# Performance work log

Measured on AMD Instinct MI355X. Metric: run time of the kernel, lower is better.

The kernel has to match this reference:

```python
import jax, jax.numpy as jnp
import numpy as np

B, T, O, D, H = 8, 256, 16, 512, 8
HD = D // H
EPS = 1e-5


def setup_inputs() -> dict:
    key = jax.random.key(0)
    ks = jax.random.split(key, 12)
    s = 1.0 / np.sqrt(D)
    inp = {
        "organ_states": jax.random.normal(ks[0], (B, T, O, D), dtype=jnp.float32),
        "organ_mask": jax.random.randint(ks[1], (B, T, O), 0, 2) > 0,
        "Wq": jax.random.uniform(ks[2], (D, D), jnp.float32, -s, s),
        "bq": jnp.zeros((D,), jnp.float32),
        "Wk": jax.random.uniform(ks[3], (D, D), jnp.float32, -s, s),
        "bk": jnp.zeros((D,), jnp.float32),
        "Wv": jax.random.uniform(ks[4], (D, D), jnp.float32, -s, s),
        "bv": jnp.zeros((D,), jnp.float32),
        "Wo": jax.random.uniform(ks[5], (D, D), jnp.float32, -s, s),
        "bo": jnp.zeros((D,), jnp.float32),
        "gamma": jnp.ones((D,), jnp.float32),
        "beta": jnp.zeros((D,), jnp.float32),
    }
    return inp


def reference(organ_states, organ_mask, Wq, bq, Wk, bk, Wv, bv, Wo, bo, gamma, beta):
    x = organ_states  # (B, T, O, D)
    b, t, o, d = x.shape

    def heads(y):  # (B,T,O,D) -> (B,O,H,T,HD)
        return y.reshape(b, t, o, H, HD).transpose(0, 2, 3, 1, 4)

    q = heads(jnp.einsum('btod,de->btoe', x, Wq) + bq)
    k = heads(jnp.einsum('btod,de->btoe', x, Wk) + bk)
    v = heads(jnp.einsum('btod,de->btoe', x, Wv) + bv)

    scores = jnp.einsum('bohqd,bohkd->bohqk', q, k) / np.sqrt(HD).astype(np.float32)
    # key mask: (B,T,O) -> (B,O,1,1,T)
    mk = organ_mask.transpose(0, 2, 1)[:, :, None, None, :]
    scores = jnp.where(mk, scores, -jnp.inf)
    attn = jax.nn.softmax(scores, axis=-1)
    attn = jnp.where(mk, attn, 0.0)

    att = jnp.einsum('bohqk,bohkd->bohqd', attn, v)  # (B,O,H,T,HD)
    att = att.transpose(0, 3, 1, 2, 4).reshape(b, t, o, d)  # (B,T,O,D)

    out = jnp.einsum('btod,de->btoe', att, Wo) + bo
    res = out + x
    mu = jnp.mean(res, axis=-1, keepdims=True)
    var = jnp.mean(jnp.square(res - mu), axis=-1, keepdims=True)
    y = (res - mu) / jnp.sqrt(var + EPS) * gamma + beta
    y = y * organ_mask[..., None].astype(y.dtype)
    return y
```

## Files before the change

kernel.cpp:

```cpp
#include <hip/hip_runtime.h>


typedef __attribute__((ext_vector_type(8))) short bf16x8;
typedef __attribute__((ext_vector_type(4))) float f32x4;

#define MFMA16(a, b, c) __builtin_amdgcn_mfma_f32_16x16x32_bf16((a), (b), (c), 0, 0, 0)

__device__ __forceinline__ unsigned short f2bf(float f) {
  unsigned int u = __builtin_bit_cast(unsigned int, f);
  u += 0x7fffu + ((u >> 16) & 1u);
  return (unsigned short)(u >> 16);
}

__device__ __forceinline__ void gload_lds16(const void* g, void* lds) {
  __builtin_amdgcn_global_load_lds((__attribute__((address_space(1))) void*)g,
                                   (__attribute__((address_space(3))) void*)lds,
                                   16, 0, 0);
}

#define WS_XB   0ull
#define WS_WT   33554432ull
#define WS_Q    35651584ull
#define WS_K    69206016ull
#define WS_V    102760448ull
#define WS_MASK 136314880ull

__global__ void k_cvt_x(const float* __restrict__ x, unsigned short* __restrict__ xb) {
  int i = blockIdx.x * 256 + threadIdx.x;
  float4 v = ((const float4*)x)[i];
  ushort4 o;
  o.x = f2bf(v.x); o.y = f2bf(v.y); o.z = f2bf(v.z); o.w = f2bf(v.w);
  ((ushort4*)xb)[i] = o;
}

__global__ void k_prep_w(const float* __restrict__ Wq, const float* __restrict__ Wk,
                         const float* __restrict__ Wv, const float* __restrict__ Wo,
                         unsigned short* __restrict__ Wt) {
  __shared__ float tl[64][65];
  const float* src = blockIdx.z == 0 ? Wq : blockIdx.z == 1 ? Wk : blockIdx.z == 2 ? Wv : Wo;
  const int d0 = blockIdx.x * 64, e0 = blockIdx.y * 64;
  const int tid = threadIdx.x;
  {
    const int dr = tid >> 2, ec = (tid & 3) * 16;
    const float4* srow = (const float4*)(src + (size_t)(d0 + dr) * 512 + e0 + ec);
#pragma unroll
    for (int j = 0; j < 4; ++j) {
      float4 v = srow[j];
      tl[dr][ec + j * 4 + 0] = v.x;
      tl[dr][ec + j * 4 + 1] = v.y;
      tl[dr][ec + j * 4 + 2] = v.z;
      tl[dr][ec + j * 4 + 3] = v.w;
    }
  }
  __syncthreads();
  const int dd0 = (tid & 7) * 8;
#pragma unroll
  for (int i = 0; i < 2; ++i) {
    int e = i * 32 + (tid >> 3);
    bf16x8 ob;
#pragma unroll
    for (int j = 0; j < 8; ++j) ob[j] = (short)f2bf(tl[dd0 + j][e]);
    *(bf16x8*)(Wt + ((size_t)blockIdx.z * 512 + e0 + e) * 512 + d0 + dd0) = ob;
  }
}

__global__ void k_prep_mask(const void* __restrict__ mraw, unsigned char* __restrict__ mout) {
  const unsigned int* u = (const unsigned int*)mraw;
  int lane = threadIdx.x & 63;
  int packed = __any(u[lane] > 1u);
  int idx = blockIdx.x * 256 + threadIdx.x;
  unsigned char m;
  if (packed) m = ((const unsigned char*)mraw)[idx] ? 1 : 0;
  else        m = u[idx] ? 1 : 0;
  mout[idx] = m;
}

__global__ __launch_bounds__(256) void k_qkv(
    const unsigned short* __restrict__ Xb, const unsigned short* __restrict__ Wt,
    const float* __restrict__ bq, const float* __restrict__ bk, const float* __restrict__ bv,
    unsigned short* __restrict__ Qb, unsigned short* __restrict__ Kb, unsigned short* __restrict__ Vb) {
  __shared__ char sm[32768];
  const int tid = threadIdx.x, l = tid & 63, w = tid >> 6;
  const int lane15 = l & 15, quad = l >> 4;
  const int flat = blockIdx.x;
  const int mtile = flat / 12, yb = flat % 12;
  const int which = yb >> 2, ntile = yb & 3;
  const int rbase = mtile * 128;
  const char* xg = (const char*)Xb + (size_t)rbase * 1024;
  const char* wgp = (const char*)(Wt + ((size_t)which * 512 + ntile * 128) * 512);
  const int wr = w >> 1, wc = w & 1;
  const int srow = tid >> 3;
  const int c16 = (tid & 7) * 16;
  char* const abase = sm;
  char* const bbase = sm + 16384;
  f32x4 acc[4][4] = {};
  for (int ks = 0; ks < 8; ++ks) {
    __syncthreads();
#pragma unroll
    for (int i = 0; i < 4; ++i) {
      int row = i * 32 + srow;
      int swz = c16 ^ ((row & 7) << 4);
      gload_lds16(xg + (size_t)row * 1024 + ks * 128 + swz, abase + i * 4096 + w * 1024);
      gload_lds16(wgp + (size_t)row * 1024 + ks * 128 + swz, bbase + i * 4096 + w * 1024);
    }
    __syncthreads();
#pragma unroll
    for (int kc = 0; kc < 2; ++kc) {
      bf16x8 af[4], bfr[4];
#pragma unroll
      for (int mt = 0; mt < 4; ++mt) {
        int row = wr * 64 + mt * 16 + lane15;
        af[mt] = *(const bf16x8*)(abase + row * 128 + ((kc * 64 + quad * 16) ^ ((row & 7) << 4)));
      }
#pragma unroll
      for (int nt = 0; nt < 4; ++nt) {
        int col = wc * 64 + nt * 16 + lane15;
        bfr[nt] = *(const bf16x8*)(bbase + col * 128 + ((kc * 64 + quad * 16) ^ ((col & 7) << 4)));
      }
#pragma unroll
      for (int mt = 0; mt < 4; ++mt)
#pragma unroll
        for (int nt = 0; nt < 4; ++nt)
          acc[mt][nt] = MFMA16(af[mt], bfr[nt], acc[mt][nt]);
    }
  }
  const float* bias = (which == 0) ? bq : (which == 1) ? bk : bv;
  unsigned short* dst = (which == 0) ? Qb : (which == 1) ? Kb : Vb;
  const int h = ntile * 2 + wc;
#pragma unroll
  for (int mt = 0; mt < 4; ++mt) {
#pragma unroll
    for (int reg = 0; reg < 4; ++reg) {
      int r = rbase + wr * 64 + mt * 16 + quad * 4 + reg;
      int b = r >> 12, t = (r >> 4) & 255, o = r & 15;
      size_t base_bt = (size_t)((b * 16 + o) * 8 + h) * 16384 + (size_t)t * 64;
#pragma unroll
      for (int nt = 0; nt < 4; ++nt) {
        int hd = nt * 16 + lane15;
        dst[base_bt + hd] = f2bf(acc[mt][nt][reg] + bias[h * 64 + hd]);
      }
    }
  }
}

__global__ __launch_bounds__(512, 2) void k_attn(
    const unsigned short* __restrict__ Qb, const unsigned short* __restrict__ Kb,
    const unsigned short* __restrict__ Vb, const unsigned char* __restrict__ Mc,
    unsigned short* __restrict__ att) {
  __shared__ char sm[99328];
  const int tid = threadIdx.x, l = tid & 63, w = tid >> 6;
  const int lane15 = l & 15, quad = l >> 4;
  const int bid = blockIdx.x;
  const int h = bid & 7, o = (bid >> 3) & 15, b = bid >> 7;
  const size_t head = (size_t)((b * 16 + o) * 8 + h) * 16384;
  const unsigned short* qh = Qb + head;
  const char* kg = (const char*)(Kb + head);
  const unsigned short* vh = Vb + head;

  {
    const int srow = tid >> 3;
    const int c16 = (tid & 7) * 16;
    char* kdst = sm + w * 1024;
#pragma unroll
    for (int i = 0; i < 4; ++i) {
      int t = i * 64 + srow;
      gload_lds16(kg + (size_t)t * 128 + (c16 ^ ((t & 7) << 4)), kdst + i * 8192);
    }
  }
  const int q0 = w * 32;
  bf16x8 qf[2][2];
#pragma unroll
  for (int mt = 0; mt < 2; ++mt)
#pragma unroll
    for (int kc = 0; kc < 2; ++kc)
      qf[mt][kc] = *(const bf16x8*)(qh + (size_t)(q0 + mt * 16 + lane15) * 64 + kc * 32 + quad * 8);
  unsigned short vreg[32];
  {
    const int hd = tid & 63, tq = tid >> 6;
#pragma unroll
    for (int i = 0; i < 4; ++i)
#pragma unroll
      for (int j = 0; j < 8; ++j)
        vreg[i * 8 + j] = vh[(size_t)(tq * 32 + i * 8 + j) * 64 + hd];
  }
  float* maskb = (float*)(sm + 98304);
  if (tid < 256)
    maskb[tid] = Mc[(size_t)(b * 256 + tid) * 16 + o] ? 0.0f : -43280.0f;
  {
    const int hd = tid & 63, tq = tid >> 6;
    const int rowb = 32768 + hd * 512;
    const int swz = (hd & 7) << 4;
#pragma unroll
    for (int i = 0; i < 4; ++i) {
      bf16x8 pk;
#pragma unroll
      for (int j = 0; j < 8; ++j) pk[j] = (short)vreg[i * 8 + j];
      int t0 = tq * 32 + i * 8;
      *(bf16x8*)(sm + rowb + ((t0 * 2) ^ swz)) = pk;
    }
  }
  __syncthreads();

  f32x4 sacc[2][16] = {};
#pragma unroll
  for (int c = 0; c < 4; ++c) {
#pragma unroll
    for (int kc = 0; kc < 2; ++kc) {
      bf16x8 kf[4];
#pragma unroll
      for (int nt = 0; nt < 4; ++nt) {
        int t = c * 64 + nt * 16 + lane15;
        int byt = t * 128 + ((kc * 64 + quad * 16) ^ ((t & 7) << 4));
        kf[nt] = *(const bf16x8*)(sm + byt);
      }
#pragma unroll
      for (int mt = 0; mt < 2; ++mt)
#pragma unroll
        for (int nt = 0; nt < 4; ++nt)
          sacc[mt][c * 4 + nt] = MFMA16(qf[mt][kc], kf[nt], sacc[mt][c * 4 + nt]);
    }
  }

  float biasv[16];
#pragma unroll
  for (int g = 0; g < 16; ++g) biasv[g] = maskb[g * 16 + lane15];
  float inv[2][4];
#pragma unroll
  for (int mt = 0; mt < 2; ++mt) {
#pragma unroll
    for (int reg = 0; reg < 4; ++reg) {
      float v[16];
#pragma unroll
      for (int g = 0; g < 16; ++g)
        v[g] = sacc[mt][g][reg] * 0.18033688f + biasv[g];
      float m = v[0];
#pragma unroll
      for (int g = 1; g < 16; ++g) m = fmaxf(m, v[g]);
#pragma unroll
      for (int d = 1; d < 16; d <<= 1) m = fmaxf(m, __shfl_xor(m, d));
      float rs = 0.f;
#pragma unroll
      for (int g = 0; g < 16; ++g) {
        float p = __builtin_amdgcn_exp2f(v[g] - m);
        sacc[mt][g][reg] = p;
        rs += p;
      }
#pragma unroll
      for (int d = 1; d < 16; d <<= 1) rs += __shfl_xor(rs, d);
      inv[mt][reg] = 1.0f / rs;
    }
  }

  char* pb = sm + 65536 + w * 4096;
  f32x4 pv[2][4] = {};
#pragma unroll
  for (int c = 0; c < 4; ++c) {
#pragma unroll
    for (int mt = 0; mt < 2; ++mt)
#pragma unroll
      for (int nt = 0; nt < 4; ++nt)
#pragma unroll
        for (int reg = 0; reg < 4; ++reg) {
          int qrow = mt * 16 + quad * 4 + reg;
          int byt = (qrow * 128 + (nt * 16 + lane15) * 2) ^ ((qrow & 7) << 4);
          *(unsigned short*)(pb + byt) = f2bf(sacc[mt][c * 4 + nt][reg]);
        }
#pragma unroll
    for (int kc = 0; kc < 2; ++kc) {
      bf16x8 pa[2], vbr[4];
#pragma unroll
      for (int mt = 0; mt < 2; ++mt) {
        int qrow = mt * 16 + lane15;
        int byt = (qrow * 128 + kc * 64 + quad * 16) ^ ((qrow & 7) << 4);
        pa[mt] = *(const bf16x8*)(pb + byt);
      }
#pragma unroll
      for (int nh = 0; nh < 4; ++nh) {
        int hd = nh * 16 + lane15;
        int byt = hd * 512 + ((c * 128 + kc * 64 + quad * 16) ^ ((hd & 7) << 4));
        vbr[nh] = *(const bf16x8*)(sm + 32768 + byt);
      }
#pragma unroll
      for (int mt = 0; mt < 2; ++mt)
#pragma unroll
        for (int nh = 0; nh < 4; ++nh)
          pv[mt][nh] = MFMA16(pa[mt], vbr[nh], pv[mt][nh]);
    }
  }

#pragma unroll
  for (int mt = 0; mt < 2; ++mt) {
#pragma unroll
    for (int reg = 0; reg < 4; ++reg) {
      int q = q0 + mt * 16 + quad * 4 + reg;
      size_t r = (size_t)(b * 256 + q) * 16 + o;
      float iv = inv[mt][reg];
#pragma unroll
      for (int nh = 0; nh < 4; ++nh)
        att[r * 512 + h * 64 + nh * 16 + lane15] = f2bf(pv[mt][nh][reg] * iv);
    }
  }
}

__global__ __launch_bounds__(512) void k_oproj(
    const unsigned short* __restrict__ A, const unsigned short* __restrict__ Wt,
    const float* __restrict__ bo, const float* __restrict__ X,
    const unsigned char* __restrict__ Mc, const float* __restrict__ gamma,
    const float* __restrict__ beta, float* __restrict__ out) {
  __shared__ char sm[73728];
  __shared__ float psum[64][8];
  __shared__ float psumsq[64][8];
  __shared__ float smean[64];
  __shared__ float srstd[64];
  const int tid = threadIdx.x, l = tid & 63, w = tid >> 6;
  const int lane15 = l & 15, quad = l >> 4;
  const int rbase = blockIdx.x * 64;
  const char* ag = (const char*)A;
  const char* wgp = (const char*)(Wt + (size_t)1536 * 512);
  const int srow = tid >> 3;
  const int c16 = (tid & 7) * 16;
  const int swz_a = c16 ^ ((srow & 7) << 4);
  char* adst = sm + w * 1024;
  f32x4 acc[4][4] = {};
  for (int ks = 0; ks < 8; ++ks) {
    __syncthreads();
    gload_lds16(ag + (size_t)(rbase + srow) * 1024 + ks * 128 + swz_a, adst);
#pragma unroll
    for (int p = 0; p < 8; ++p) {
      int er = p * 64 + srow;
      gload_lds16(wgp + (size_t)er * 1024 + ks * 128 + (c16 ^ ((er & 7) << 4)),
                  sm + 8192 + p * 8192 + w * 1024);
    }
    __syncthreads();
#pragma unroll
    for (int kc = 0; kc < 2; ++kc) {
      bf16x8 af[4], bfr[4];
#pragma unroll
      for (int mt = 0; mt < 4; ++mt) {
        int row = mt * 16 + lane15;
        int byt = (row * 128 + kc * 64 + quad * 16) ^ ((row & 7) << 4);
        af[mt] = *(const bf16x8*)(sm + byt);
      }
#pragma unroll
      for (int nt = 0; nt < 4; ++nt) {
        int col = w * 64 + nt * 16 + lane15;
        int byt = (col * 128 + kc * 64 + quad * 16) ^ ((col & 7) << 4);
        bfr[nt] = *(const bf16x8*)(sm + 8192 + byt);
      }
#pragma unroll
      for (int mt = 0; mt < 4; ++mt)
#pragma unroll
        for (int nt = 0; nt < 4; ++nt)
          acc[mt][nt] = MFMA16(af[mt], bfr[nt], acc[mt][nt]);
    }
  }
#pragma unroll
  for (int mt = 0; mt < 4; ++mt) {
#pragma unroll
    for (int reg = 0; reg < 4; ++reg) {
      int rl = mt * 16 + quad * 4 + reg;
      int r = rbase + rl;
      float s1 = 0.f, s2 = 0.f;
#pragma unroll
      for (int nt = 0; nt < 4; ++nt) {
        int col = w * 64 + nt * 16 + lane15;
        float v = acc[mt][nt][reg] + bo[col] + X[(size_t)r * 512 + col];
        acc[mt][nt][reg] = v;
        s1 += v; s2 += v * v;
      }
#pragma unroll
      for (int d = 1; d < 16; d <<= 1) { s1 += __shfl_xor(s1, d); s2 += __shfl_xor(s2, d); }
      if (lane15 == 0) { psum[rl][w] = s1; psumsq[rl][w] = s2; }
    }
  }
  __syncthreads();
  if (tid < 64) {
    float a = 0.f, q = 0.f;
#pragma unroll
    for (int j = 0; j < 8; ++j) { a += psum[tid][j]; q += psumsq[tid][j]; }
    float mu = a * (1.f / 512.f);
    float var = q * (1.f / 512.f) - mu * mu;
    smean[tid] = mu;
    srstd[tid] = rsqrtf(fmaxf(var, 0.f) + 1e-5f);
  }
  __syncthreads();
#pragma unroll
  for (int mt = 0; mt < 4; ++mt) {
#pragma unroll
    for (int reg = 0; reg < 4; ++reg) {
      int rl = mt * 16 + quad * 4 + reg;
      int r = rbase + rl;
      float mu = smean[rl], rs = srstd[rl];
      float mkf = Mc[r] ? 1.f : 0.f;
#pragma unroll
      for (int nt = 0; nt < 4; ++nt) {
        int col = w * 64 + nt * 16 + lane15;
        float y = (acc[mt][nt][reg] - mu) * rs * gamma[col] + beta[col];
        out[(size_t)r * 512 + col] = y * mkf;
      }
    }
  }
}

extern "C" void kernel_launch(void* const* d_in, const int* in_sizes, int n_in,
                              void* d_out, int out_size, void* d_ws, size_t ws_size,
                              hipStream_t stream) {
  const float* X     = (const float*)d_in[0];
  const void*  Mraw  = d_in[1];
  const float* Wq    = (const float*)d_in[2];
  const float* bq    = (const float*)d_in[3];
  const float* Wk    = (const float*)d_in[4];
  const float* bk    = (const float*)d_in[5];
  const float* Wv    = (const float*)d_in[6];
  const float* bv    = (const float*)d_in[7];
  const float* Wo    = (const float*)d_in[8];
  const float* bo    = (const float*)d_in[9];
  const float* gamma = (const float*)d_in[10];
  const float* beta  = (const float*)d_in[11];

  char* ws = (char*)d_ws;
  unsigned short* Xb  = (unsigned short*)(ws + WS_XB);
  unsigned short* Wt  = (unsigned short*)(ws + WS_WT);
  unsigned short* Qb  = (unsigned short*)(ws + WS_Q);
  unsigned short* Kb  = (unsigned short*)(ws + WS_K);
  unsigned short* Vb  = (unsigned short*)(ws + WS_V);
  unsigned char*  Mc  = (unsigned char*)(ws + WS_MASK);
  unsigned short* att = Xb;

  hipLaunchKernelGGL(k_cvt_x,    dim3(16384),   dim3(256), 0, stream, X, Xb);
  hipLaunchKernelGGL(k_prep_w,   dim3(8, 8, 4), dim3(256), 0, stream, Wq, Wk, Wv, Wo, Wt);
  hipLaunchKernelGGL(k_prep_mask,dim3(128),     dim3(256), 0, stream, Mraw, Mc);
  hipLaunchKernelGGL(k_qkv,      dim3(3072),    dim3(256), 0, stream, Xb, Wt, bq, bk, bv, Qb, Kb, Vb);
  hipLaunchKernelGGL(k_attn,     dim3(1024),    dim3(512), 0, stream, Qb, Kb, Vb, Mc, att);
  hipLaunchKernelGGL(k_oproj,    dim3(512),     dim3(512), 0, stream, att, Wt, bo, X, Mc, gamma, beta,
                     (float*)d_out);
}
```

Before: 297.5 us.

## Merge prep kernels, double-buffer 128x512 GEMM tiles, add MFMA priority hints

The three prep kernels become one launch that picks its role from the block index. The QKV and output projections now share a macro GEMM core with 1024-thread blocks. Each block covers 128 rows by the full 512 columns, double-buffers LDS stages and uses explicit vmcnt waits so global loads overlap compute. The attention kernel reuses the K region for the P buffer to shrink LDS and raises wave priority around the MFMA loops. In exchange, the 160KB LDS per block limits occupancy to one block per CU, and the projection grids become much smaller (768 and 256 blocks).

Measured after the change: 300.6 us. About the same (+1.0%).

```diff
diff --git a/kernel.cpp b/kernel.cpp
--- a/kernel.cpp
+++ b/kernel.cpp
@@ -25,119 +25,139 @@
 #define WS_V    102760448ull
 #define WS_MASK 136314880ull
 
-__global__ void k_cvt_x(const float* __restrict__ x, unsigned short* __restrict__ xb) {
-  int i = blockIdx.x * 256 + threadIdx.x;
-  float4 v = ((const float4*)x)[i];
-  ushort4 o;
-  o.x = f2bf(v.x); o.y = f2bf(v.y); o.z = f2bf(v.z); o.w = f2bf(v.w);
-  ((ushort4*)xb)[i] = o;
-}
-
-__global__ void k_prep_w(const float* __restrict__ Wq, const float* __restrict__ Wk,
-                         const float* __restrict__ Wv, const float* __restrict__ Wo,
-                         unsigned short* __restrict__ Wt) {
+__global__ void k_prep(const float* __restrict__ x, unsigned short* __restrict__ xb,
+                       const float* __restrict__ Wq, const float* __restrict__ Wk,
+                       const float* __restrict__ Wv, const float* __restrict__ Wo,
+                       unsigned short* __restrict__ Wt,
+                       const void* __restrict__ mraw, unsigned char* __restrict__ mout) {
   __shared__ float tl[64][65];
-  const float* src = blockIdx.z == 0 ? Wq : blockIdx.z == 1 ? Wk : blockIdx.z == 2 ? Wv : Wo;
-  const int d0 = blockIdx.x * 64, e0 = blockIdx.y * 64;
-  const int tid = threadIdx.x;
-  {
-    const int dr = tid >> 2, ec = (tid & 3) * 16;
-    const float4* srow = (const float4*)(src + (size_t)(d0 + dr) * 512 + e0 + ec);
-#pragma unroll
-    for (int j = 0; j < 4; ++j) {
-      float4 v = srow[j];
-      tl[dr][ec + j * 4 + 0] = v.x;
-      tl[dr][ec + j * 4 + 1] = v.y;
-      tl[dr][ec + j * 4 + 2] = v.z;
-      tl[dr][ec + j * 4 + 3] = v.w;
-    }
-  }
-  __syncthreads();
-  const int dd0 = (tid & 7) * 8;
-#pragma unroll
-  for (int i = 0; i < 2; ++i) {
-    int e = i * 32 + (tid >> 3);
-    bf16x8 ob;
-#pragma unroll
-    for (int j = 0; j < 8; ++j) ob[j] = (short)f2bf(tl[dd0 + j][e]);
-    *(bf16x8*)(Wt + ((size_t)blockIdx.z * 512 + e0 + e) * 512 + d0 + dd0) = ob;
-  }
-}
-
-__global__ void k_prep_mask(const void* __restrict__ mraw, unsigned char* __restrict__ mout) {
-  const unsigned int* u = (const unsigned int*)mraw;
-  int lane = threadIdx.x & 63;
-  int packed = __any(u[lane] > 1u);
-  int idx = blockIdx.x * 256 + threadIdx.x;
-  unsigned char m;
-  if (packed) m = ((const unsigned char*)mraw)[idx] ? 1 : 0;
-  else        m = u[idx] ? 1 : 0;
-  mout[idx] = m;
-}
-
-__global__ __launch_bounds__(256) void k_qkv(
+  const int bid = blockIdx.x, tid = threadIdx.x;
+  if (bid < 16384) {
+    int i = bid * 256 + tid;
+    float4 v = ((const float4*)x)[i];
+    ushort4 o;
+    o.x = f2bf(v.x); o.y = f2bf(v.y); o.z = f2bf(v.z); o.w = f2bf(v.w);
+    ((ushort4*)xb)[i] = o;
+  } else if (bid < 16640) {
+    int p = bid - 16384;
+    int which = p >> 6, rem = p & 63, dt = rem >> 3, et = rem & 7;
+    const float* src = which == 0 ? Wq : which == 1 ? Wk : which == 2 ? Wv : Wo;
+    const int d0 = dt * 64, e0 = et * 64;
+    {
+      const int dr = tid >> 2, ec = (tid & 3) * 16;
+      const float4* srow = (const float4*)(src + (size_t)(d0 + dr) * 512 + e0 + ec);
+#pragma unroll
+      for (int j = 0; j < 4; ++j) {
+        float4 v = srow[j];
+        tl[dr][ec + j * 4 + 0] = v.x;
+        tl[dr][ec + j * 4 + 1] = v.y;
+        tl[dr][ec + j * 4 + 2] = v.z;
+        tl[dr][ec + j * 4 + 3] = v.w;
+      }
+    }
+    __syncthreads();
+    const int dd0 = (tid & 7) * 8;
+#pragma unroll
+    for (int i = 0; i < 2; ++i) {
+      int e = i * 32 + (tid >> 3);
+      bf16x8 ob;
+#pragma unroll
+      for (int j = 0; j < 8; ++j) ob[j] = (short)f2bf(tl[dd0 + j][e]);
+      *(bf16x8*)(Wt + ((size_t)which * 512 + e0 + e) * 512 + d0 + dd0) = ob;
+    }
+  } else {
+    int p = bid - 16640;
+    const unsigned int* u = (const unsigned int*)mraw;
+    int lane = tid & 63;
+    int packed = __any(u[lane] > 1u);
+    int idx = p * 256 + tid;
+    unsigned char m;
+    if (packed) m = ((const unsigned char*)mraw)[idx] ? 1 : 0;
+    else        m = u[idx] ? 1 : 0;
+    mout[idx] = m;
+  }
+}
+
+#define GEMM_CORE(AG, WG)                                                                 \
+  const int tid = threadIdx.x, l = tid & 63;                                              \
+  const int lane15 = l & 15, quad = l >> 4;                                               \
+  const int w = tid >> 6, wr = w >> 3, wc = w & 7;                                        \
+  const int srow = tid >> 3;                                                              \
+  const int c16 = (tid & 7) * 16;                                                         \
+  auto STAGE = [&](int ks, char* buf) {                                                   \
+    { int row = srow;                                                                     \
+      gload_lds16((AG) + (size_t)(rbase + row) * 1024 + ks * 128 + (c16 ^ ((row & 7) << 4)),\
+                  buf + tid * 16); }                                                      \
+    _Pragma("unroll")                                                                     \
+    for (int i = 0; i < 4; ++i) {                                                         \
+      int row = i * 128 + srow;                                                           \
+      gload_lds16((WG) + (size_t)row * 1024 + ks * 128 + (c16 ^ ((row & 7) << 4)),        \
+                  buf + 16384 + i * 16384 + tid * 16);                                    \
+    }                                                                                     \
+  };                                                                                      \
+  f32x4 acc[4][4] = {};                                                                   \
+  STAGE(0, sm);                                                                           \
+  STAGE(1, sm + 81920);                                                                   \
+  asm volatile("s_waitcnt vmcnt(5)" ::: "memory");                                        \
+  __builtin_amdgcn_sched_barrier(0);                                                      \
+  __builtin_amdgcn_s_barrier();                                                           \
+  for (int ks = 0; ks < 8; ++ks) {                                                        \
+    char* cur = sm + (ks & 1) * 81920;                                                    \
+    _Pragma("unroll")                                                                     \
+    for (int kc = 0; kc < 2; ++kc) {                                                      \
+      bf16x8 af[4], bfr[4];                                                               \
+      _Pragma("unroll")                                                                   \
+      for (int mt = 0; mt < 4; ++mt) {                                                    \
+        int row = wr * 64 + mt * 16 + lane15;                                             \
+        af[mt] = *(const bf16x8*)(cur + row * 128 + ((kc * 64 + quad * 16) ^ ((row & 7) << 4))); \
+      }                                                                                   \
+      _Pragma("unroll")                                                                   \
+      for (int nt = 0; nt < 4; ++nt) {                                                    \
+        int col = wc * 64 + nt * 16 + lane15;                                             \
+        bfr[nt] = *(const bf16x8*)(cur + 16384 + col * 128 + ((kc * 64 + quad * 16) ^ ((col & 7) << 4))); \
+      }                                                                                   \
+      _Pragma("unroll")                                                                   \
+      for (int mt = 0; mt < 4; ++mt)                                                      \
+        _Pragma("unroll")                                                                 \
+        for (int nt = 0; nt < 4; ++nt)                                                    \
+          acc[mt][nt] = MFMA16(af[mt], bfr[nt], acc[mt][nt]);                             \
+    }                                                                                     \
+    if (ks == 7) break;                                                                   \
+    __builtin_amdgcn_s_barrier();                    \
+    if (ks < 6) {                                                                         \
+      STAGE(ks + 2, sm + (ks & 1) * 81920);                                               \
+      asm volatile("s_waitcnt vmcnt(5)" ::: "memory");              \
+    } else {                                                                              \
+      asm volatile("s_waitcnt vmcnt(0)" ::: "memory");                                    \
+    }                                                                                     \
+    __builtin_amdgcn_sched_barrier(0);                                                    \
+    __builtin_amdgcn_s_barrier();                                                         \
+  }
+
+__global__ __launch_bounds__(1024) void k_qkv(
     const unsigned short* __restrict__ Xb, const unsigned short* __restrict__ Wt,
     const float* __restrict__ bq, const float* __restrict__ bk, const float* __restrict__ bv,
     unsigned short* __restrict__ Qb, unsigned short* __restrict__ Kb, unsigned short* __restrict__ Vb) {
-  __shared__ char sm[32768];
-  const int tid = threadIdx.x, l = tid & 63, w = tid >> 6;
-  const int lane15 = l & 15, quad = l >> 4;
+  __shared__ char sm[163840];
   const int flat = blockIdx.x;
-  const int mtile = flat / 12, yb = flat % 12;
-  const int which = yb >> 2, ntile = yb & 3;
+  const int mtile = flat / 3, which = flat % 3;
   const int rbase = mtile * 128;
-  const char* xg = (const char*)Xb + (size_t)rbase * 1024;
-  const char* wgp = (const char*)(Wt + ((size_t)which * 512 + ntile * 128) * 512);
-  const int wr = w >> 1, wc = w & 1;
-  const int srow = tid >> 3;
-  const int c16 = (tid & 7) * 16;
-  char* const abase = sm;
-  char* const bbase = sm + 16384;
-  f32x4 acc[4][4] = {};
-  for (int ks = 0; ks < 8; ++ks) {
-    __syncthreads();
-#pragma unroll
-    for (int i = 0; i < 4; ++i) {
-      int row = i * 32 + srow;
-      int swz = c16 ^ ((row & 7) << 4);
-      gload_lds16(xg + (size_t)row * 1024 + ks * 128 + swz, abase + i * 4096 + w * 1024);
-      gload_lds16(wgp + (size_t)row * 1024 + ks * 128 + swz, bbase + i * 4096 + w * 1024);
-    }
-    __syncthreads();
-#pragma unroll
-    for (int kc = 0; kc < 2; ++kc) {
-      bf16x8 af[4], bfr[4];
-#pragma unroll
-      for (int mt = 0; mt < 4; ++mt) {
-        int row = wr * 64 + mt * 16 + lane15;
-        af[mt] = *(const bf16x8*)(abase + row * 128 + ((kc * 64 + quad * 16) ^ ((row & 7) << 4)));
-      }
-#pragma unroll
-      for (int nt = 0; nt < 4; ++nt) {
-        int col = wc * 64 + nt * 16 + lane15;
-        bfr[nt] = *(const bf16x8*)(bbase + col * 128 + ((kc * 64 + quad * 16) ^ ((col & 7) << 4)));
-      }
-#pragma unroll
-      for (int mt = 0; mt < 4; ++mt)
-#pragma unroll
-        for (int nt = 0; nt < 4; ++nt)
-          acc[mt][nt] = MFMA16(af[mt], bfr[nt], acc[mt][nt]);
-    }
-  }
+  const char* ag = (const char*)Xb;
+  const char* wg = (const char*)(Wt + (size_t)which * 512 * 512);
+  GEMM_CORE(ag, wg)
   const float* bias = (which == 0) ? bq : (which == 1) ? bk : bv;
   unsigned short* dst = (which == 0) ? Qb : (which == 1) ? Kb : Vb;
-  const int h = ntile * 2 + wc;
 #pragma unroll
   for (int mt = 0; mt < 4; ++mt) {
 #pragma unroll
     for (int reg = 0; reg < 4; ++reg) {
       int r = rbase + wr * 64 + mt * 16 + quad * 4 + reg;
       int b = r >> 12, t = (r >> 4) & 255, o = r & 15;
-      size_t base_bt = (size_t)((b * 16 + o) * 8 + h) * 16384 + (size_t)t * 64;
+      size_t base_bt = (size_t)((b * 16 + o) * 8 + wc) * 16384 + (size_t)t * 64;
 #pragma unroll
       for (int nt = 0; nt < 4; ++nt) {
         int hd = nt * 16 + lane15;
-        dst[base_bt + hd] = f2bf(acc[mt][nt][reg] + bias[h * 64 + hd]);
+        dst[base_bt + hd] = f2bf(acc[mt][nt][reg] + bias[wc * 64 + hd]);
       }
     }
   }
@@ -147,7 +167,7 @@
     const unsigned short* __restrict__ Qb, const unsigned short* __restrict__ Kb,
     const unsigned short* __restrict__ Vb, const unsigned char* __restrict__ Mc,
     unsigned short* __restrict__ att) {
-  __shared__ char sm[99328];
+  __shared__ char sm[66560];
   const int tid = threadIdx.x, l = tid & 63, w = tid >> 6;
   const int lane15 = l & 15, quad = l >> 4;
   const int bid = blockIdx.x;
@@ -183,7 +203,7 @@
       for (int j = 0; j < 8; ++j)
         vreg[i * 8 + j] = vh[(size_t)(tq * 32 + i * 8 + j) * 64 + hd];
   }
-  float* maskb = (float*)(sm + 98304);
+  float* maskb = (float*)(sm + 65536);
   if (tid < 256)
     maskb[tid] = Mc[(size_t)(b * 256 + tid) * 16 + o] ? 0.0f : -43280.0f;
   {
@@ -202,6 +222,7 @@
   __syncthreads();
 
   f32x4 sacc[2][16] = {};
+  __builtin_amdgcn_s_setprio(1);
 #pragma unroll
   for (int c = 0; c < 4; ++c) {
 #pragma unroll
@@ -220,6 +241,8 @@
           sacc[mt][c * 4 + nt] = MFMA16(qf[mt][kc], kf[nt], sacc[mt][c * 4 + nt]);
     }
   }
+  __builtin_amdgcn_s_setprio(0);
+  __syncthreads();
 
   float biasv[16];
 #pragma unroll
@@ -251,7 +274,7 @@
     }
   }
 
-  char* pb = sm + 65536 + w * 4096;
+  char* pb = sm + w * 4096;
   f32x4 pv[2][4] = {};
 #pragma unroll
   for (int c = 0; c < 4; ++c) {
@@ -265,6 +288,7 @@
           int byt = (qrow * 128 + (nt * 16 + lane15) * 2) ^ ((qrow & 7) << 4);
           *(unsigned short*)(pb + byt) = f2bf(sacc[mt][c * 4 + nt][reg]);
         }
+    __builtin_amdgcn_s_setprio(1);
 #pragma unroll
     for (int kc = 0; kc < 2; ++kc) {
       bf16x8 pa[2], vbr[4];
@@ -286,6 +310,7 @@
         for (int nh = 0; nh < 4; ++nh)
           pv[mt][nh] = MFMA16(pa[mt], vbr[nh], pv[mt][nh]);
     }
+    __builtin_amdgcn_s_setprio(0);
   }
 
 #pragma unroll
@@ -302,82 +327,45 @@
   }
 }
 
-__global__ __launch_bounds__(512) void k_oproj(
+__global__ __launch_bounds__(1024) void k_oproj(
     const unsigned short* __restrict__ A, const unsigned short* __restrict__ Wt,
     const float* __restrict__ bo, const float* __restrict__ X,
     const unsigned char* __restrict__ Mc, const float* __restrict__ gamma,
     const float* __restrict__ beta, float* __restrict__ out) {
-  __shared__ char sm[73728];
-  __shared__ float psum[64][8];
-  __shared__ float psumsq[64][8];
-  __shared__ float smean[64];
-  __shared__ float srstd[64];
-  const int tid = threadIdx.x, l = tid & 63, w = tid >> 6;
-  const int lane15 = l & 15, quad = l >> 4;
-  const int rbase = blockIdx.x * 64;
+  __shared__ char sm[163840];
+  const int rbase = blockIdx.x * 128;
   const char* ag = (const char*)A;
-  const char* wgp = (const char*)(Wt + (size_t)1536 * 512);
-  const int srow = tid >> 3;
-  const int c16 = (tid & 7) * 16;
-  const int swz_a = c16 ^ ((srow & 7) << 4);
-  char* adst = sm + w * 1024;
-  f32x4 acc[4][4] = {};
-  for (int ks = 0; ks < 8; ++ks) {
-    __syncthreads();
-    gload_lds16(ag + (size_t)(rbase + srow) * 1024 + ks * 128 + swz_a, adst);
-#pragma unroll
-    for (int p = 0; p < 8; ++p) {
-      int er = p * 64 + srow;
-      gload_lds16(wgp + (size_t)er * 1024 + ks * 128 + (c16 ^ ((er & 7) << 4)),
-                  sm + 8192 + p * 8192 + w * 1024);
-    }
-    __syncthreads();
-#pragma unroll
-    for (int kc = 0; kc < 2; ++kc) {
-      bf16x8 af[4], bfr[4];
-#pragma unroll
-      for (int mt = 0; mt < 4; ++mt) {
-        int row = mt * 16 + lane15;
-        int byt = (row * 128 + kc * 64 + quad * 16) ^ ((row & 7) << 4);
-        af[mt] = *(const bf16x8*)(sm + byt);
-      }
-#pragma unroll
-      for (int nt = 0; nt < 4; ++nt) {
-        int col = w * 64 + nt * 16 + lane15;
-        int byt = (col * 128 + kc * 64 + quad * 16) ^ ((col & 7) << 4);
-        bfr[nt] = *(const bf16x8*)(sm + 8192 + byt);
-      }
-#pragma unroll
-      for (int mt = 0; mt < 4; ++mt)
-#pragma unroll
-        for (int nt = 0; nt < 4; ++nt)
-          acc[mt][nt] = MFMA16(af[mt], bfr[nt], acc[mt][nt]);
-    }
-  }
+  const char* wg = (const char*)(Wt + (size_t)1536 * 512);
+  GEMM_CORE(ag, wg)
+  float* psum   = (float*)sm;
+  float* psumsq = (float*)(sm + 4096);
+  float* smean  = (float*)(sm + 8192);
+  float* srstd  = (float*)(sm + 8704);
+  __syncthreads();
 #pragma unroll
   for (int mt = 0; mt < 4; ++mt) {
 #pragma unroll
     for (int reg = 0; reg < 4; ++reg) {
-      int rl = mt * 16 + quad * 4 + reg;
+      int rl = wr * 64 + mt * 16 + quad * 4 + reg;
       int r = rbase + rl;
       float s1 = 0.f, s2 = 0.f;
 #pragma unroll
       for (int nt = 0; nt < 4; ++nt) {
-        int col = w * 64 + nt * 16 + lane15;
+        int col = wc * 64 + nt * 16 + lane15;
         float v = acc[mt][nt][reg] + bo[col] + X[(size_t)r * 512 + col];
         acc[mt][nt][reg] = v;
         s1 += v; s2 += v * v;
       }
 #pragma unroll
       for (int d = 1; d < 16; d <<= 1) { s1 += __shfl_xor(s1, d); s2 += __shfl_xor(s2, d); }
-      if (lane15 == 0) { psum[rl][w] = s1; psumsq[rl][w] = s2; }
+      if (lane15 == 0) { psum[rl * 8 + wc] = s1; psumsq[rl * 8 + wc] = s2; }
     }
   }
   __syncthreads();
-  if (tid < 64) {
+  if (tid < 128) {
     float a = 0.f, q = 0.f;
 #pragma unroll
-    for (int j = 0; j < 8; ++j) { a += psum[tid][j]; q += psumsq[tid][j]; }
+    for (int j = 0; j < 8; ++j) { a += psum[tid * 8 + j]; q += psumsq[tid * 8 + j]; }
     float mu = a * (1.f / 512.f);
     float var = q * (1.f / 512.f) - mu * mu;
     smean[tid] = mu;
@@ -388,13 +376,13 @@
   for (int mt = 0; mt < 4; ++mt) {
 #pragma unroll
     for (int reg = 0; reg < 4; ++reg) {
-      int rl = mt * 16 + quad * 4 + reg;
+      int rl = wr * 64 + mt * 16 + quad * 4 + reg;
       int r = rbase + rl;
       float mu = smean[rl], rs = srstd[rl];
       float mkf = Mc[r] ? 1.f : 0.f;
 #pragma unroll
       for (int nt = 0; nt < 4; ++nt) {
-        int col = w * 64 + nt * 16 + lane15;
+        int col = wc * 64 + nt * 16 + lane15;
         float y = (acc[mt][nt][reg] - mu) * rs * gamma[col] + beta[col];
         out[(size_t)r * 512 + col] = y * mkf;
       }
@@ -427,11 +415,10 @@
   unsigned char*  Mc  = (unsigned char*)(ws + WS_MASK);
   unsigned short* att = Xb;
 
-  hipLaunchKernelGGL(k_cvt_x,    dim3(16384),   dim3(256), 0, stream, X, Xb);
-  hipLaunchKernelGGL(k_prep_w,   dim3(8, 8, 4), dim3(256), 0, stream, Wq, Wk, Wv, Wo, Wt);
-  hipLaunchKernelGGL(k_prep_mask,dim3(128),     dim3(256), 0, stream, Mraw, Mc);
-  hipLaunchKernelGGL(k_qkv,      dim3(3072),    dim3(256), 0, stream, Xb, Wt, bq, bk, bv, Qb, Kb, Vb);
-  hipLaunchKernelGGL(k_attn,     dim3(1024),    dim3(512), 0, stream, Qb, Kb, Vb, Mc, att);
-  hipLaunchKernelGGL(k_oproj,    dim3(512),     dim3(512), 0, stream, att, Wt, bo, X, Mc, gamma, beta,
+  hipLaunchKernelGGL(k_prep,  dim3(16768), dim3(256), 0, stream,
+                     X, Xb, Wq, Wk, Wv, Wo, Wt, Mraw, Mc);
+  hipLaunchKernelGGL(k_qkv,   dim3(768),   dim3(1024), 0, stream, Xb, Wt, bq, bk, bv, Qb, Kb, Vb);
+  hipLaunchKernelGGL(k_attn,  dim3(1024),  dim3(512), 0, stream, Qb, Kb, Vb, Mc, att);
+  hipLaunchKernelGGL(k_oproj, dim3(256),   dim3(1024), 0, stream, att, Wt, bo, X, Mc, gamma, beta,
                      (float*)d_out);
 }
```
